# Kernel tuning notes

Hardware: AMD Instinct MI355X
Metric: run time of the kernel (lower is better)

Reference implementation:

```python
import jax, jax.numpy as jnp
import numpy as np

# Cost coefficients from MatcherConfig (init_kwargs)
C_CLASS, C_MASK, C_DICE, C_DIST, C_NLL, C_LIK = 2.0, 5.0, 5.0, 1.0, 0.5, 0.5

B, P, Q, E = 8, 16384, 256, 128  # images, pixels (H*W), queries, electrons


def setup_inputs() -> dict:
    key = jax.random.key(0)
    ks = jax.random.split(key, 8)
    mask_mask = jax.random.uniform(ks[0], (B, P, Q)) < 0.10           # sparsity pattern of pred logits
    mask_logit_values = jax.random.normal(ks[1], (B, P, Q), jnp.float32)
    seg_occ = jax.random.uniform(ks[2], (B, P, E)) < 0.05              # sparsity pattern of target segmap
    seg_vals = jax.random.uniform(ks[3], (B, P, E), jnp.float32, 1e-3, 1.0)
    segmap_values = jnp.where(seg_occ, seg_vals, 0.0)
    pred_logits = jax.random.normal(ks[4], (B, Q), jnp.float32)
    pred_positions = jax.random.uniform(ks[5], (B, Q, 2), jnp.float32)
    true_positions = jax.random.uniform(ks[6], (B, E, 2), jnp.float32)
    kd, ko = jax.random.split(ks[7])
    diag = 1.0 + 2.0 * jax.random.uniform(kd, (B, Q, 2), jnp.float32)  # positive diag of scale_tril
    off = 0.3 * jax.random.normal(ko, (B, Q), jnp.float32)
    pred_chol = jnp.zeros((B, Q, 2, 2), jnp.float32)
    pred_chol = pred_chol.at[..., 0, 0].set(diag[..., 0])
    pred_chol = pred_chol.at[..., 1, 1].set(diag[..., 1])
    pred_chol = pred_chol.at[..., 1, 0].set(off)
    image_sizes_xy = jnp.full((B, 2), 128.0, jnp.float32)
    return {
        'pred_logits': pred_logits,
        'mask_logit_values': mask_logit_values,
        'mask_mask': mask_mask,
        'segmap_values': segmap_values,
        'pred_positions': pred_positions,
        'pred_chol': pred_chol,
        'true_positions': true_positions,
        'image_sizes_xy': image_sizes_xy,
    }


def _total_cost(pred_logits, mask_logit_values, segmap_values, pred_positions,
                pred_chol, true_positions, image_sizes_xy, mask_mask):
    sp = jax.nn.softplus
    m = mask_mask
    # --- class cost: BCE(logit, 1) per query -> [B,Q]
    class_cost = sp(-pred_logits)
    # --- mask BCE cost (get_bce_cost): sparse entries only
    pos = jnp.where(m, sp(-mask_logit_values), 0.0)   # BCE vs 1 on nnz entries
    neg = jnp.where(m, sp(mask_logit_values), 0.0)    # BCE vs 0 on nnz entries
    targ = (segmap_values > 0).astype(pos.dtype)      # binarized target segmap
    pos_loss = jnp.einsum('bpq,bpe->bqe', pos, targ)
    neg_loss = neg.sum(1)[:, :, None] - jnp.einsum('bpq,bpe->bqe', neg, targ)
    nnz = jnp.maximum(targ.sum((1, 2)), 1.0)          # target _nnz() per image
    mask_cost = (pos_loss + neg_loss) / nnz[:, None, None]
    # --- dice cost (get_dice_cost): sparse softmax over query dim
    NEG = jnp.asarray(-1e30, mask_logit_values.dtype)
    z = jnp.where(m, mask_logit_values, NEG)
    mx = jnp.max(z, axis=-1, keepdims=True)
    ez = jnp.where(m, jnp.exp(z - mx), 0.0)
    s = ez.sum(-1, keepdims=True)
    pred_p = jnp.where(s > 0, ez / jnp.maximum(s, 1e-30), 0.0)  # [B,P,Q]
    num = 2.0 * jnp.einsum('bpq,bpe->bqe', pred_p, segmap_values)
    den = pred_p.sum(1)[:, :, None] + segmap_values.sum(1)[:, None, :]
    dice_cost = 1.0 - (num + 1.0) / (den + 1.0)
    # --- huber distance cost (delta=1), mean over xy
    d = pred_positions[:, :, None, :] - true_positions[:, None, :, :]  # [B,Q,E,2]
    ad = jnp.abs(d)
    huber_cost = jnp.where(ad < 1.0, 0.5 * d * d, ad - 0.5).mean(-1)
    # --- NLL / likelihood distance costs (MVN with scale_tril)
    mu = pred_positions * image_sizes_xy[:, None, :]
    y = true_positions * image_sizes_xy[:, None, :]
    diff = y[:, None, :, :] - mu[:, :, None, :]        # [B,Q,E,2]
    L00 = pred_chol[..., 0, 0][:, :, None]
    L10 = pred_chol[..., 1, 0][:, :, None]
    L11 = pred_chol[..., 1, 1][:, :, None]
    z0 = diff[..., 0] / L00
    z1 = (diff[..., 1] - L10 * z0) / L11
    nll_cost = 0.5 * (z0 * z0 + z1 * z1) + jnp.log(2.0 * jnp.pi) + jnp.log(L00) + jnp.log(L11)
    lik_cost = 1.0 - jnp.exp(-nll_cost)
    total = (C_CLASS * class_cost[:, :, None] + C_MASK * mask_cost + C_DICE * dice_cost
             + C_DIST * huber_cost + C_NLL * nll_cost + C_LIK * lik_cost)
    return total  # [B, Q, E] stacked per-image cost matrices


def reference(pred_logits, mask_logit_values, mask_mask, segmap_values,
              pred_positions, pred_chol, true_positions, image_sizes_xy):
    return _total_cost(pred_logits, mask_logit_values, segmap_values, pred_positions,
                       pred_chol, true_positions, image_sizes_xy, mask_mask)
```

## Files before the change

### kernel.cpp

```cpp
#include <hip/hip_runtime.h>
#include <cstdint>
#include <cstddef>

typedef float v4f __attribute__((ext_vector_type(4)));
typedef short short8 __attribute__((ext_vector_type(8)));

constexpr int B_ = 8, P_ = 16384, Q_ = 256, E_ = 128;

__device__ __forceinline__ unsigned short f2bf(float f) {
  unsigned int x = __float_as_uint(f);
  x += 0x7FFFu + ((x >> 16) & 1u);
  return (unsigned short)(x >> 16);
}
__device__ __forceinline__ float softplus_f(float x) {
  return fmaxf(x, 0.f) + __logf(1.f + __expf(-fabsf(x)));
}

__global__ __launch_bounds__(256) void prep_rows(
    const float* __restrict__ mlv, const int* __restrict__ mask,
    unsigned short* __restrict__ A1, unsigned short* __restrict__ PP,
    float* __restrict__ negsum, float* __restrict__ ppsum)
{
  __shared__ float rn[4][256];
  __shared__ float rp[4][256];
  const int t = threadIdx.x, w = t >> 6, l = t & 63;
  const int b = blockIdx.x >> 7;
  float accN[4] = {0,0,0,0}, accP[4] = {0,0,0,0};
  for (int it = 0; it < 32; ++it) {
    const size_t row = (size_t)blockIdx.x * 128 + it * 4 + w;
    const size_t off = row * 256 + l * 4;
    float4 x4 = *(const float4*)(mlv + off);
    int4   m4 = *(const int4*)(mask + off);
    float xs[4] = {x4.x, x4.y, x4.z, x4.w};
    int   ms[4] = {m4.x, m4.y, m4.z, m4.w};
    float ez[4]; float s = 0.f;
    unsigned short a1u[4];
#pragma unroll
    for (int j = 0; j < 4; ++j) {
      bool m = (ms[j] != 0);
      float x = xs[j];
      float e = m ? __expf(x) : 0.f;
      ez[j] = e; s += e;
      a1u[j] = f2bf(m ? -x : 0.f);
      accN[j] += m ? softplus_f(x) : 0.f;
    }
#pragma unroll
    for (int o = 32; o > 0; o >>= 1) s += __shfl_xor(s, o, 64);
    float inv = (s > 0.f) ? (1.f / s) : 0.f;
    unsigned short pu[4];
#pragma unroll
    for (int j = 0; j < 4; ++j) { float p = ez[j] * inv; accP[j] += p; pu[j] = f2bf(p); }
    uint2 aw, pw;
    aw.x = (unsigned)a1u[0] | ((unsigned)a1u[1] << 16);
    aw.y = (unsigned)a1u[2] | ((unsigned)a1u[3] << 16);
    pw.x = (unsigned)pu[0] | ((unsigned)pu[1] << 16);
    pw.y = (unsigned)pu[2] | ((unsigned)pu[3] << 16);
    *(uint2*)(A1 + off) = aw;
    *(uint2*)(PP + off) = pw;
  }
#pragma unroll
  for (int j = 0; j < 4; ++j) { rn[w][l * 4 + j] = accN[j]; rp[w][l * 4 + j] = accP[j]; }
  __syncthreads();
  float sn = rn[0][t] + rn[1][t] + rn[2][t] + rn[3][t];
  float sq = rp[0][t] + rp[1][t] + rp[2][t] + rp[3][t];
  atomicAdd(&negsum[b * 256 + t], sn);
  atomicAdd(&ppsum[b * 256 + t], sq);
}

__global__ __launch_bounds__(256) void prep_seg(
    const float* __restrict__ seg, unsigned short* __restrict__ SG,
    float* __restrict__ segsum, float* __restrict__ nnzb)
{
  __shared__ float sbin[128];
  __shared__ float nns;
  const int t = threadIdx.x;
  const int b = blockIdx.x >> 6;
  if (t < 128) sbin[t] = 0.f;
  if (t == 0) nns = 0.f;
  __syncthreads();
  float accS[4] = {0,0,0,0}; float cnt = 0.f;
  const size_t base = (size_t)blockIdx.x * 32768 + t * 4;
  for (int it = 0; it < 32; ++it) {
    size_t off = base + (size_t)it * 1024;
    float4 v = *(const float4*)(seg + off);
    float vs[4] = {v.x, v.y, v.z, v.w};
    unsigned short u[4];
#pragma unroll
    for (int j = 0; j < 4; ++j) {
      u[j] = f2bf(vs[j]); accS[j] += vs[j];
      cnt += (vs[j] > 0.f) ? 1.f : 0.f;
    }
    uint2 wv; wv.x = (unsigned)u[0] | ((unsigned)u[1] << 16);
    wv.y = (unsigned)u[2] | ((unsigned)u[3] << 16);
    *(uint2*)(SG + off) = wv;
  }
  const int e0 = (t * 4) & 127;
#pragma unroll
  for (int j = 0; j < 4; ++j) atomicAdd(&sbin[e0 + j], accS[j]);
#pragma unroll
  for (int o = 32; o > 0; o >>= 1) cnt += __shfl_xor(cnt, o, 64);
  if ((t & 63) == 0) atomicAdd(&nns, cnt);
  __syncthreads();
  if (t < 128) atomicAdd(&segsum[b * 128 + t], sbin[t]);
  if (t == 0) atomicAdd(&nnzb[b], nns);
}

__global__ __launch_bounds__(256) void gemm_split(
    const unsigned short* __restrict__ A1, const unsigned short* __restrict__ PP,
    const unsigned short* __restrict__ SG, float* __restrict__ part)
{
  __shared__ __align__(16) unsigned int ldsA[128 * 36];
  __shared__ __align__(16) unsigned int ldsB[128 * 36];
  const int id = blockIdx.x;
  const int ks = id & 15, qt = (id >> 4) & 1, g = (id >> 5) & 1, b = id >> 6;
  const unsigned short* Aop = (g ? PP : A1) + (size_t)b * P_ * Q_;
  const unsigned short* Bop = SG + (size_t)b * P_ * E_;
  const int t = threadIdx.x;
  const int c16 = t >> 4, pr = t & 15;
  const int w = t >> 6, l = t & 63, lm = l & 15, quad = l >> 4;
  const int wm = w & 1, wn = w >> 1;
  v4f acc[4][4];
#pragma unroll
  for (int i = 0; i < 4; ++i)
#pragma unroll
    for (int j = 0; j < 4; ++j) acc[i][j] = (v4f)0.f;

  for (int c = 0; c < 16; ++c) {
    const int pbase = ks * 1024 + c * 64;
    __syncthreads();
#pragma unroll
    for (int pass = 0; pass < 2; ++pass) {
      const int r0 = pass * 32 + 2 * pr;
      const unsigned short* ap = Aop + (size_t)(pbase + r0) * Q_ + qt * 128 + c16 * 8;
      uint4 w0 = *(const uint4*)ap;
      uint4 w1 = *(const uint4*)(ap + Q_);
      const unsigned short* bp = Bop + (size_t)(pbase + r0) * E_ + c16 * 8;
      uint4 v0 = *(const uint4*)bp;
      uint4 v1 = *(const uint4*)(bp + E_);
      const int dbase = pass * 16 + pr;
      unsigned int aw0[4] = {w0.x, w0.y, w0.z, w0.w};
      unsigned int aw1[4] = {w1.x, w1.y, w1.z, w1.w};
      unsigned int bw0[4] = {v0.x, v0.y, v0.z, v0.w};
      unsigned int bw1[4] = {v1.x, v1.y, v1.z, v1.w};
#pragma unroll
      for (int k = 0; k < 4; ++k) {
        const int col = c16 * 8 + 2 * k;
        unsigned int lo = (aw0[k] & 0xFFFFu) | (aw1[k] << 16);
        unsigned int hi = (aw0[k] >> 16) | (aw1[k] & 0xFFFF0000u);
        ldsA[col * 36 + dbase] = lo;
        ldsA[(col + 1) * 36 + dbase] = hi;
        unsigned int blo = (bw0[k] & 0xFFFFu) | (bw1[k] << 16);
        unsigned int bhi = (bw0[k] >> 16) | (bw1[k] & 0xFFFF0000u);
        if (g == 0) {
          blo = ((blo & 0xFFFFu) ? 0x3F80u : 0u) | ((blo & 0xFFFF0000u) ? 0x3F800000u : 0u);
          bhi = ((bhi & 0xFFFFu) ? 0x3F80u : 0u) | ((bhi & 0xFFFF0000u) ? 0x3F800000u : 0u);
        }
        ldsB[col * 36 + dbase] = blo;
        ldsB[(col + 1) * 36 + dbase] = bhi;
      }
    }
    __syncthreads();
#pragma unroll
    for (int k32 = 0; k32 < 2; ++k32) {
      short8 af[4], bf[4];
#pragma unroll
      for (int i = 0; i < 4; ++i) {
        const int arow = wm * 64 + i * 16 + lm;
        af[i] = *(const short8*)((const char*)ldsA + arow * 144 + k32 * 64 + quad * 16);
        const int brow = wn * 64 + i * 16 + lm;
        bf[i] = *(const short8*)((const char*)ldsB + brow * 144 + k32 * 64 + quad * 16);
      }
#pragma unroll
      for (int i = 0; i < 4; ++i)
#pragma unroll
        for (int j = 0; j < 4; ++j)
          acc[i][j] = __builtin_amdgcn_mfma_f32_16x16x32_bf16(af[i], bf[j], acc[i][j], 0, 0, 0);
    }
  }
  float* pout = part + ((size_t)(g * 8 + b) * 16 + ks) * (Q_ * E_);
#pragma unroll
  for (int i = 0; i < 4; ++i)
#pragma unroll
    for (int r = 0; r < 4; ++r) {
      const int q = qt * 128 + wm * 64 + i * 16 + quad * 4 + r;
#pragma unroll
      for (int j = 0; j < 4; ++j) {
        const int e = wn * 64 + j * 16 + lm;
        pout[q * E_ + e] = acc[i][j][r];
      }
    }
}

__global__ __launch_bounds__(128) void epilogue(
    const float* __restrict__ part,
    const float* __restrict__ negsum, const float* __restrict__ ppsum,
    const float* __restrict__ segsum, const float* __restrict__ nnzb,
    const float* __restrict__ logits, const float* __restrict__ ppos,
    const float* __restrict__ chol, const float* __restrict__ tpos,
    const float* __restrict__ imgsz, float* __restrict__ out)
{
  const int bq = blockIdx.x;
  const int b = bq >> 8;
  const int e = threadIdx.x;
  const int qe = (bq & 255) * 128 + e;
  const float* p0 = part + (size_t)b * 524288 + qe;
  const float* p1 = part + (size_t)(8 + b) * 524288 + qe;
  float g1 = 0.f, g2 = 0.f;
#pragma unroll
  for (int k = 0; k < 16; ++k) { g1 += p0[k * 32768]; g2 += p1[k * 32768]; }

  const float nnz = fmaxf(nnzb[b], 1.f);
  const float mask_cost = (negsum[bq] + g1) / nnz;
  const float dice = 1.f - (2.f * g2 + 1.f) / (ppsum[bq] + segsum[b * 128 + e] + 1.f);
  const float cls = softplus_f(-logits[bq]);
  const float px = ppos[bq * 2], py = ppos[bq * 2 + 1];
  const float tx = tpos[(b * 128 + e) * 2], ty = tpos[(b * 128 + e) * 2 + 1];
  const float dx = px - tx, dy = py - ty;
  const float ax = fabsf(dx), ay = fabsf(dy);
  const float hx = (ax < 1.f) ? 0.5f * dx * dx : ax - 0.5f;
  const float hy = (ay < 1.f) ? 0.5f * dy * dy : ay - 0.5f;
  const float huber = 0.5f * (hx + hy);
  const float sx = imgsz[b * 2], sy = imgsz[b * 2 + 1];
  const float L00 = chol[bq * 4 + 0], L10 = chol[bq * 4 + 2], L11 = chol[bq * 4 + 3];
  const float d0 = (tx - px) * sx, d1 = (ty - py) * sy;
  const float z0 = d0 / L00;
  const float z1 = (d1 - L10 * z0) / L11;
  const float nll = 0.5f * (z0 * z0 + z1 * z1) + 1.8378770664093453f + __logf(L00) + __logf(L11);
  const float lik = 1.f - __expf(-nll);
  out[bq * 128 + e] = 2.f * cls + 5.f * mask_cost + 5.f * dice + huber + 0.5f * nll + 0.5f * lik;
}

extern "C" void kernel_launch(void* const* d_in, const int* in_sizes, int n_in,
                              void* d_out, int out_size, void* d_ws, size_t ws_size,
                              hipStream_t stream)
{
  (void)in_sizes; (void)n_in; (void)out_size; (void)ws_size;
  const float* logits = (const float*)d_in[0];
  const float* mlv    = (const float*)d_in[1];
  const int*   mask   = (const int*)d_in[2];
  const float* seg    = (const float*)d_in[3];
  const float* ppos   = (const float*)d_in[4];
  const float* chol   = (const float*)d_in[5];
  const float* tpos   = (const float*)d_in[6];
  const float* imgsz  = (const float*)d_in[7];

  char* ws = (char*)d_ws;
  unsigned short* A1 = (unsigned short*)(ws);
  unsigned short* PP = (unsigned short*)(ws + 67108864);
  unsigned short* SG = (unsigned short*)(ws + 134217728);
  float* part   = (float*)(ws + 167772160);
  float* negsum = (float*)(ws + 234881024);
  float* ppsum  = (float*)(ws + 234889216);
  float* segsum = (float*)(ws + 234897408);
  float* nnzb   = (float*)(ws + 234901504);

  hipMemsetAsync(ws + 234881024, 0, 20544, stream);
  prep_rows<<<1024, 256, 0, stream>>>(mlv, mask, A1, PP, negsum, ppsum);
  prep_seg<<<512, 256, 0, stream>>>(seg, SG, segsum, nnzb);
  gemm_split<<<512, 256, 0, stream>>>(A1, PP, SG, part);
  epilogue<<<2048, 128, 0, stream>>>(part, negsum, ppsum, segsum, nnzb,
                                     logits, ppos, chol, tpos, imgsz, (float*)d_out);
}
```

Before: 425.6 us.

## Pre-transpose bf16 operands into swizzled tiles and load GEMM tiles directly to LDS

The prep kernels now write A, P, segmap and a precomputed binary segmap as K-major swizzled 64-pixel tiles, transposed through LDS. This lets the GEMM fill shared memory with direct global-to-LDS 16-byte loads, with no in-kernel shuffling or binarisation. The split-K partial outputs are summed with atomics into one buffer, so the epilogue no longer reads 16 partial slices. The cost is an extra binary segmap buffer, atomic contention in the GEMM store, and a more complex prep transpose with larger register arrays.

```diff
diff --git a/kernel.cpp b/kernel.cpp
--- a/kernel.cpp
+++ b/kernel.cpp
@@ -4,171 +4,254 @@
 
 typedef float v4f __attribute__((ext_vector_type(4)));
 typedef short short8 __attribute__((ext_vector_type(8)));
+typedef unsigned short ushort_t;
 
 constexpr int B_ = 8, P_ = 16384, Q_ = 256, E_ = 128;
 
-__device__ __forceinline__ unsigned short f2bf(float f) {
+__device__ __forceinline__ unsigned int f2bf(float f) {
   unsigned int x = __float_as_uint(f);
   x += 0x7FFFu + ((x >> 16) & 1u);
-  return (unsigned short)(x >> 16);
+  return x >> 16;
 }
 __device__ __forceinline__ float softplus_f(float x) {
   return fmaxf(x, 0.f) + __logf(1.f + __expf(-fabsf(x)));
 }
-
-__global__ __launch_bounds__(256) void prep_rows(
+__device__ __forceinline__ void gload16(const void* g, void* l) {
+  __builtin_amdgcn_global_load_lds((const __attribute__((address_space(1))) void*)g,
+                                   (__attribute__((address_space(3))) void*)l,
+                                   16, 0, 0);
+}
+
+__global__ __launch_bounds__(256, 4) void prep_rows(
     const float* __restrict__ mlv, const int* __restrict__ mask,
-    unsigned short* __restrict__ A1, unsigned short* __restrict__ PP,
+    ushort_t* __restrict__ A1T, ushort_t* __restrict__ PPT,
     float* __restrict__ negsum, float* __restrict__ ppsum)
 {
-  __shared__ float rn[4][256];
-  __shared__ float rp[4][256];
+  __shared__ unsigned int st[256 * 33];
   const int t = threadIdx.x, w = t >> 6, l = t & 63;
-  const int b = blockIdx.x >> 7;
-  float accN[4] = {0,0,0,0}, accP[4] = {0,0,0,0};
-  for (int it = 0; it < 32; ++it) {
-    const size_t row = (size_t)blockIdx.x * 128 + it * 4 + w;
-    const size_t off = row * 256 + l * 4;
-    float4 x4 = *(const float4*)(mlv + off);
-    int4   m4 = *(const int4*)(mask + off);
-    float xs[4] = {x4.x, x4.y, x4.z, x4.w};
-    int   ms[4] = {m4.x, m4.y, m4.z, m4.w};
-    float ez[4]; float s = 0.f;
-    unsigned short a1u[4];
+  const int b = blockIdx.x >> 8, cp = blockIdx.x & 255;
+  const size_t base = ((size_t)b * P_ + cp * 64) * Q_;
+  float accN[4] = {0.f,0.f,0.f,0.f}, accP[4] = {0.f,0.f,0.f,0.f};
+  unsigned int a1w[4][4][2], ppw[4][4][2];
+
+#pragma unroll
+  for (int g = 0; g < 4; ++g) {
+#pragma unroll
+    for (int j = 0; j < 4; ++j) { a1w[g][j][0]=0; a1w[g][j][1]=0; ppw[g][j][0]=0; ppw[g][j][1]=0; }
+#pragma unroll
+    for (int r = 0; r < 4; ++r) {
+      const int pl = (w << 4) + (g << 2) + r;
+      const float* xp = mlv + base + (size_t)pl * Q_ + l;
+      const int*   mp = mask + base + (size_t)pl * Q_ + l;
+      float xs[4]; int ms[4];
+#pragma unroll
+      for (int j = 0; j < 4; ++j) { xs[j] = xp[j * 64]; ms[j] = mp[j * 64]; }
+      float ev[4]; float s = 0.f;
+#pragma unroll
+      for (int j = 0; j < 4; ++j) {
+        const bool mm = ms[j] != 0;
+        const float xv = xs[j];
+        const float e = mm ? __expf(xv) : 0.f;
+        ev[j] = e; s += e;
+        accN[j] += __logf(1.f + e);
+        a1w[g][j][r >> 1] |= f2bf(mm ? -xv : 0.f) << ((r & 1) * 16);
+      }
+#pragma unroll
+      for (int o = 32; o; o >>= 1) s += __shfl_xor(s, o, 64);
+      const float inv = (s > 0.f) ? (1.f / s) : 0.f;
+#pragma unroll
+      for (int j = 0; j < 4; ++j) {
+        const float p = ev[j] * inv;
+        accP[j] += p;
+        ppw[g][j][r >> 1] |= f2bf(p) << ((r & 1) * 16);
+      }
+    }
+  }
+  const size_t tb = ((size_t)(b * 256 + cp)) * 16384;
+#pragma unroll
+  for (int g = 0; g < 4; ++g)
 #pragma unroll
     for (int j = 0; j < 4; ++j) {
-      bool m = (ms[j] != 0);
-      float x = xs[j];
-      float e = m ? __expf(x) : 0.f;
-      ez[j] = e; s += e;
-      a1u[j] = f2bf(m ? -x : 0.f);
-      accN[j] += m ? softplus_f(x) : 0.f;
-    }
-#pragma unroll
-    for (int o = 32; o > 0; o >>= 1) s += __shfl_xor(s, o, 64);
-    float inv = (s > 0.f) ? (1.f / s) : 0.f;
-    unsigned short pu[4];
-#pragma unroll
-    for (int j = 0; j < 4; ++j) { float p = ez[j] * inv; accP[j] += p; pu[j] = f2bf(p); }
-    uint2 aw, pw;
-    aw.x = (unsigned)a1u[0] | ((unsigned)a1u[1] << 16);
-    aw.y = (unsigned)a1u[2] | ((unsigned)a1u[3] << 16);
-    pw.x = (unsigned)pu[0] | ((unsigned)pu[1] << 16);
-    pw.y = (unsigned)pu[2] | ((unsigned)pu[3] << 16);
-    *(uint2*)(A1 + off) = aw;
-    *(uint2*)(PP + off) = pw;
-  }
-#pragma unroll
-  for (int j = 0; j < 4; ++j) { rn[w][l * 4 + j] = accN[j]; rp[w][l * 4 + j] = accP[j]; }
-  __syncthreads();
-  float sn = rn[0][t] + rn[1][t] + rn[2][t] + rn[3][t];
-  float sq = rp[0][t] + rp[1][t] + rp[2][t] + rp[3][t];
-  atomicAdd(&negsum[b * 256 + t], sn);
-  atomicAdd(&ppsum[b * 256 + t], sq);
-}
-
-__global__ __launch_bounds__(256) void prep_seg(
-    const float* __restrict__ seg, unsigned short* __restrict__ SG,
+      const int wb = (l + (j << 6)) * 33 + (w << 3) + (g << 1);
+      st[wb] = a1w[g][j][0]; st[wb + 1] = a1w[g][j][1];
+    }
+  __syncthreads();
+  {
+    uint4* dst = (uint4*)(A1T + tb);
+#pragma unroll
+    for (int pass = 0; pass < 8; ++pass) {
+      const int gi = pass * 256 + t;
+      const int q = gi >> 3, c = (gi & 7) ^ (q & 7);
+      const int wd = q * 33 + c * 4;
+      uint4 v; v.x = st[wd]; v.y = st[wd+1]; v.z = st[wd+2]; v.w = st[wd+3];
+      dst[gi] = v;
+    }
+  }
+  __syncthreads();
+#pragma unroll
+  for (int g = 0; g < 4; ++g)
+#pragma unroll
+    for (int j = 0; j < 4; ++j) {
+      const int wb = (l + (j << 6)) * 33 + (w << 3) + (g << 1);
+      st[wb] = ppw[g][j][0]; st[wb + 1] = ppw[g][j][1];
+    }
+  __syncthreads();
+  {
+    uint4* dst = (uint4*)(PPT + tb);
+#pragma unroll
+    for (int pass = 0; pass < 8; ++pass) {
+      const int gi = pass * 256 + t;
+      const int q = gi >> 3, c = (gi & 7) ^ (q & 7);
+      const int wd = q * 33 + c * 4;
+      uint4 v; v.x = st[wd]; v.y = st[wd+1]; v.z = st[wd+2]; v.w = st[wd+3];
+      dst[gi] = v;
+    }
+  }
+  __syncthreads();
+  float* red = (float*)st;
+#pragma unroll
+  for (int j = 0; j < 4; ++j) red[w * 256 + l + (j << 6)] = accN[j];
+  __syncthreads();
+  {
+    const float sn = red[t] + red[256 + t] + red[512 + t] + red[768 + t];
+    atomicAdd(&negsum[b * 256 + t], sn);
+  }
+  __syncthreads();
+#pragma unroll
+  for (int j = 0; j < 4; ++j) red[w * 256 + l + (j << 6)] = accP[j];
+  __syncthreads();
+  {
+    const float sq = red[t] + red[256 + t] + red[512 + t] + red[768 + t];
+    atomicAdd(&ppsum[b * 256 + t], sq);
+  }
+}
+
+__global__ __launch_bounds__(256, 4) void prep_seg(
+    const float* __restrict__ seg, ushort_t* __restrict__ SGT, ushort_t* __restrict__ SGB,
     float* __restrict__ segsum, float* __restrict__ nnzb)
 {
-  __shared__ float sbin[128];
-  __shared__ float nns;
-  const int t = threadIdx.x;
-  const int b = blockIdx.x >> 6;
-  if (t < 128) sbin[t] = 0.f;
-  if (t == 0) nns = 0.f;
-  __syncthreads();
-  float accS[4] = {0,0,0,0}; float cnt = 0.f;
-  const size_t base = (size_t)blockIdx.x * 32768 + t * 4;
-  for (int it = 0; it < 32; ++it) {
-    size_t off = base + (size_t)it * 1024;
-    float4 v = *(const float4*)(seg + off);
-    float vs[4] = {v.x, v.y, v.z, v.w};
-    unsigned short u[4];
-#pragma unroll
-    for (int j = 0; j < 4; ++j) {
-      u[j] = f2bf(vs[j]); accS[j] += vs[j];
-      cnt += (vs[j] > 0.f) ? 1.f : 0.f;
-    }
-    uint2 wv; wv.x = (unsigned)u[0] | ((unsigned)u[1] << 16);
-    wv.y = (unsigned)u[2] | ((unsigned)u[3] << 16);
-    *(uint2*)(SG + off) = wv;
-  }
-  const int e0 = (t * 4) & 127;
-#pragma unroll
-  for (int j = 0; j < 4; ++j) atomicAdd(&sbin[e0 + j], accS[j]);
-#pragma unroll
-  for (int o = 32; o > 0; o >>= 1) cnt += __shfl_xor(cnt, o, 64);
-  if ((t & 63) == 0) atomicAdd(&nns, cnt);
-  __syncthreads();
-  if (t < 128) atomicAdd(&segsum[b * 128 + t], sbin[t]);
-  if (t == 0) atomicAdd(&nnzb[b], nns);
-}
-
-__global__ __launch_bounds__(256) void gemm_split(
-    const unsigned short* __restrict__ A1, const unsigned short* __restrict__ PP,
-    const unsigned short* __restrict__ SG, float* __restrict__ part)
-{
-  __shared__ __align__(16) unsigned int ldsA[128 * 36];
-  __shared__ __align__(16) unsigned int ldsB[128 * 36];
+  __shared__ unsigned int st[128 * 33];
+  const int t = threadIdx.x, w = t >> 6, l = t & 63;
+  const int b = blockIdx.x >> 8, cp = blockIdx.x & 255;
+  const size_t base = ((size_t)b * P_ + cp * 64) * E_;
+  float accS[2] = {0.f, 0.f}; float cnt = 0.f;
+  unsigned int sgw[4][2][2], sbw[4][2][2];
+#pragma unroll
+  for (int g = 0; g < 4; ++g) {
+#pragma unroll
+    for (int j = 0; j < 2; ++j) { sgw[g][j][0]=0; sgw[g][j][1]=0; sbw[g][j][0]=0; sbw[g][j][1]=0; }
+#pragma unroll
+    for (int r = 0; r < 4; ++r) {
+      const int pl = (w << 4) + (g << 2) + r;
+      const float* vp = seg + base + (size_t)pl * E_ + l;
+#pragma unroll
+      for (int j = 0; j < 2; ++j) {
+        const float v = vp[j * 64];
+        const bool nz = v > 0.f;
+        accS[j] += v; cnt += nz ? 1.f : 0.f;
+        sgw[g][j][r >> 1] |= f2bf(v) << ((r & 1) * 16);
+        sbw[g][j][r >> 1] |= (nz ? 0x3F80u : 0u) << ((r & 1) * 16);
+      }
+    }
+  }
+  const size_t tb = ((size_t)(b * 256 + cp)) * 8192;
+#pragma unroll
+  for (int g = 0; g < 4; ++g)
+#pragma unroll
+    for (int j = 0; j < 2; ++j) {
+      const int wb = (l + (j << 6)) * 33 + (w << 3) + (g << 1);
+      st[wb] = sgw[g][j][0]; st[wb + 1] = sgw[g][j][1];
+    }
+  __syncthreads();
+  {
+    uint4* dst = (uint4*)(SGT + tb);
+#pragma unroll
+    for (int pass = 0; pass < 4; ++pass) {
+      const int gi = pass * 256 + t;
+      const int q = gi >> 3, c = (gi & 7) ^ (q & 7);
+      const int wd = q * 33 + c * 4;
+      uint4 v; v.x = st[wd]; v.y = st[wd+1]; v.z = st[wd+2]; v.w = st[wd+3];
+      dst[gi] = v;
+    }
+  }
+  __syncthreads();
+#pragma unroll
+  for (int g = 0; g < 4; ++g)
+#pragma unroll
+    for (int j = 0; j < 2; ++j) {
+      const int wb = (l + (j << 6)) * 33 + (w << 3) + (g << 1);
+      st[wb] = sbw[g][j][0]; st[wb + 1] = sbw[g][j][1];
+    }
+  __syncthreads();
+  {
+    uint4* dst = (uint4*)(SGB + tb);
+#pragma unroll
+    for (int pass = 0; pass < 4; ++pass) {
+      const int gi = pass * 256 + t;
+      const int q = gi >> 3, c = (gi & 7) ^ (q & 7);
+      const int wd = q * 33 + c * 4;
+      uint4 v; v.x = st[wd]; v.y = st[wd+1]; v.z = st[wd+2]; v.w = st[wd+3];
+      dst[gi] = v;
+    }
+  }
+  __syncthreads();
+  float* red = (float*)st;
+#pragma unroll
+  for (int j = 0; j < 2; ++j) red[w * 128 + l + (j << 6)] = accS[j];
+  __syncthreads();
+  if (t < 128) {
+    const float ss = red[t] + red[128 + t] + red[256 + t] + red[384 + t];
+    atomicAdd(&segsum[b * 128 + t], ss);
+  }
+#pragma unroll
+  for (int o = 32; o; o >>= 1) cnt += __shfl_xor(cnt, o, 64);
+  if (l == 0) atomicAdd(&nnzb[b], cnt);
+}
+
+__global__ __launch_bounds__(256, 2) void gemm_mfma(
+    const ushort_t* __restrict__ A1T, const ushort_t* __restrict__ PPT,
+    const ushort_t* __restrict__ SGT, const ushort_t* __restrict__ SGB,
+    float* __restrict__ part)
+{
+  __shared__ __align__(16) char lds[32768];
   const int id = blockIdx.x;
   const int ks = id & 15, qt = (id >> 4) & 1, g = (id >> 5) & 1, b = id >> 6;
-  const unsigned short* Aop = (g ? PP : A1) + (size_t)b * P_ * Q_;
-  const unsigned short* Bop = SG + (size_t)b * P_ * E_;
-  const int t = threadIdx.x;
-  const int c16 = t >> 4, pr = t & 15;
-  const int w = t >> 6, l = t & 63, lm = l & 15, quad = l >> 4;
+  const ushort_t* Aall = g ? PPT : A1T;
+  const ushort_t* Ball = g ? SGT : SGB;
+  const int t = threadIdx.x, l = t & 63, w = t >> 6;
+  const int lm = l & 15, quad = l >> 4;
   const int wm = w & 1, wn = w >> 1;
   v4f acc[4][4];
 #pragma unroll
   for (int i = 0; i < 4; ++i)
 #pragma unroll
     for (int j = 0; j < 4; ++j) acc[i][j] = (v4f)0.f;
-
-  for (int c = 0; c < 16; ++c) {
-    const int pbase = ks * 1024 + c * 64;
+  const size_t cp0 = (size_t)b * 256 + ks * 16;
+  const char* gA = (const char*)(Aall + cp0 * 16384 + qt * 8192);
+  const char* gB = (const char*)(Ball + cp0 * 8192);
+  const int off = t * 16;
+
+  for (int it = 0; it < 16; ++it) {
     __syncthreads();
-#pragma unroll
-    for (int pass = 0; pass < 2; ++pass) {
-      const int r0 = pass * 32 + 2 * pr;
-      const unsigned short* ap = Aop + (size_t)(pbase + r0) * Q_ + qt * 128 + c16 * 8;
-      uint4 w0 = *(const uint4*)ap;
-      uint4 w1 = *(const uint4*)(ap + Q_);
-      const unsigned short* bp = Bop + (size_t)(pbase + r0) * E_ + c16 * 8;
-      uint4 v0 = *(const uint4*)bp;
-      uint4 v1 = *(const uint4*)(bp + E_);
-      const int dbase = pass * 16 + pr;
-      unsigned int aw0[4] = {w0.x, w0.y, w0.z, w0.w};
-      unsigned int aw1[4] = {w1.x, w1.y, w1.z, w1.w};
-      unsigned int bw0[4] = {v0.x, v0.y, v0.z, v0.w};
-      unsigned int bw1[4] = {v1.x, v1.y, v1.z, v1.w};
-#pragma unroll
-      for (int k = 0; k < 4; ++k) {
-        const int col = c16 * 8 + 2 * k;
-        unsigned int lo = (aw0[k] & 0xFFFFu) | (aw1[k] << 16);
-        unsigned int hi = (aw0[k] >> 16) | (aw1[k] & 0xFFFF0000u);
-        ldsA[col * 36 + dbase] = lo;
-        ldsA[(col + 1) * 36 + dbase] = hi;
-        unsigned int blo = (bw0[k] & 0xFFFFu) | (bw1[k] << 16);
-        unsigned int bhi = (bw0[k] >> 16) | (bw1[k] & 0xFFFF0000u);
-        if (g == 0) {
-          blo = ((blo & 0xFFFFu) ? 0x3F80u : 0u) | ((blo & 0xFFFF0000u) ? 0x3F800000u : 0u);
-          bhi = ((bhi & 0xFFFFu) ? 0x3F80u : 0u) | ((bhi & 0xFFFF0000u) ? 0x3F800000u : 0u);
-        }
-        ldsB[col * 36 + dbase] = blo;
-        ldsB[(col + 1) * 36 + dbase] = bhi;
-      }
-    }
+    const char* pa = gA + (size_t)it * 32768;
+    const char* pb = gB + (size_t)it * 16384;
+    gload16(pa + off,          lds + off);
+    gload16(pa + off + 4096,   lds + off + 4096);
+    gload16(pa + off + 8192,   lds + off + 8192);
+    gload16(pa + off + 12288,  lds + off + 12288);
+    gload16(pb + off,          lds + 16384 + off);
+    gload16(pb + off + 4096,   lds + 16384 + off + 4096);
+    gload16(pb + off + 8192,   lds + 16384 + off + 8192);
+    gload16(pb + off + 12288,  lds + 16384 + off + 12288);
     __syncthreads();
 #pragma unroll
     for (int k32 = 0; k32 < 2; ++k32) {
       short8 af[4], bf[4];
+      const int ach = ((k32 << 2) | quad) ^ (lm & 7);
 #pragma unroll
       for (int i = 0; i < 4; ++i) {
-        const int arow = wm * 64 + i * 16 + lm;
-        af[i] = *(const short8*)((const char*)ldsA + arow * 144 + k32 * 64 + quad * 16);
-        const int brow = wn * 64 + i * 16 + lm;
-        bf[i] = *(const short8*)((const char*)ldsB + brow * 144 + k32 * 64 + quad * 16);
+        af[i] = *(const short8*)(lds + (wm * 64 + i * 16 + lm) * 128 + ach * 16);
+        bf[i] = *(const short8*)(lds + 16384 + (wn * 64 + i * 16 + lm) * 128 + ach * 16);
       }
 #pragma unroll
       for (int i = 0; i < 4; ++i)
@@ -177,7 +260,7 @@
           acc[i][j] = __builtin_amdgcn_mfma_f32_16x16x32_bf16(af[i], bf[j], acc[i][j], 0, 0, 0);
     }
   }
-  float* pout = part + ((size_t)(g * 8 + b) * 16 + ks) * (Q_ * E_);
+  float* pout = part + (size_t)(g * 8 + b) * 32768;
 #pragma unroll
   for (int i = 0; i < 4; ++i)
 #pragma unroll
@@ -186,7 +269,7 @@
 #pragma unroll
       for (int j = 0; j < 4; ++j) {
         const int e = wn * 64 + j * 16 + lm;
-        pout[q * E_ + e] = acc[i][j][r];
+        atomicAdd(&pout[q * 128 + e], acc[i][j][r]);
       }
     }
 }
@@ -203,11 +286,8 @@
   const int b = bq >> 8;
   const int e = threadIdx.x;
   const int qe = (bq & 255) * 128 + e;
-  const float* p0 = part + (size_t)b * 524288 + qe;
-  const float* p1 = part + (size_t)(8 + b) * 524288 + qe;
-  float g1 = 0.f, g2 = 0.f;
-#pragma unroll
-  for (int k = 0; k < 16; ++k) { g1 += p0[k * 32768]; g2 += p1[k * 32768]; }
+  const float g1 = part[(size_t)b * 32768 + qe];
+  const float g2 = part[(size_t)(8 + b) * 32768 + qe];
 
   const float nnz = fmaxf(nnzb[b], 1.f);
   const float mask_cost = (negsum[bq] + g1) / nnz;
@@ -245,19 +325,20 @@
   const float* imgsz  = (const float*)d_in[7];
 
   char* ws = (char*)d_ws;
-  unsigned short* A1 = (unsigned short*)(ws);
-  unsigned short* PP = (unsigned short*)(ws + 67108864);
-  unsigned short* SG = (unsigned short*)(ws + 134217728);
-  float* part   = (float*)(ws + 167772160);
-  float* negsum = (float*)(ws + 234881024);
-  float* ppsum  = (float*)(ws + 234889216);
-  float* segsum = (float*)(ws + 234897408);
-  float* nnzb   = (float*)(ws + 234901504);
-
-  hipMemsetAsync(ws + 234881024, 0, 20544, stream);
-  prep_rows<<<1024, 256, 0, stream>>>(mlv, mask, A1, PP, negsum, ppsum);
-  prep_seg<<<512, 256, 0, stream>>>(seg, SG, segsum, nnzb);
-  gemm_split<<<512, 256, 0, stream>>>(A1, PP, SG, part);
+  ushort_t* A1T = (ushort_t*)(ws);
+  ushort_t* PPT = (ushort_t*)(ws + 67108864);
+  ushort_t* SGT = (ushort_t*)(ws + 134217728);
+  ushort_t* SGB = (ushort_t*)(ws + 167772160);
+  float* part   = (float*)(ws + 201326592);
+  float* negsum = (float*)(ws + 203423744);
+  float* ppsum  = (float*)(ws + 203431936);
+  float* segsum = (float*)(ws + 203440128);
+  float* nnzb   = (float*)(ws + 203444224);
+
+  hipMemsetAsync(ws + 201326592, 0, 2117696, stream);
+  prep_seg<<<2048, 256, 0, stream>>>(seg, SGT, SGB, segsum, nnzb);
+  prep_rows<<<2048, 256, 0, stream>>>(mlv, mask, A1T, PPT, negsum, ppsum);
+  gemm_mfma<<<512, 256, 0, stream>>>(A1T, PPT, SGT, SGB, part);
   epilogue<<<2048, 128, 0, stream>>>(part, negsum, ppsum, segsum, nnzb,
                                      logits, ppos, chol, tpos, imgsz, (float*)d_out);
 }
```

Result: slower. 512.6 us (+20.4%).

## Fuse prep and GEMM into one kernel, reducing split-K partials with atomics

Applied to the files above, without the earlier changes.

Merges the row-softmax/BCE prep, segmap prep and both bf16 MFMA GEMMs into a single kernel. Each block converts its pixel slab to bf16 directly in LDS and multiplies there, so the bf16 intermediates (A1, PP, SG) are never written to or read back from global memory. Split-K partials are now combined with float atomics into one small buffer, so the epilogue reads one value instead of summing 16. The softplus term is computed as log(1+exp(x)) from the already-computed exponential. Costs: only 256 blocks of 512 threads, a large atomic epilogue, and a serialized convert-then-MFMA loop with two barriers per step.

```diff
diff --git a/kernel.cpp b/kernel.cpp
--- a/kernel.cpp
+++ b/kernel.cpp
@@ -7,186 +7,207 @@
 
 constexpr int B_ = 8, P_ = 16384, Q_ = 256, E_ = 128;
 
-__device__ __forceinline__ unsigned short f2bf(float f) {
+__device__ __forceinline__ unsigned int f2bf(float f) {
   unsigned int x = __float_as_uint(f);
   x += 0x7FFFu + ((x >> 16) & 1u);
-  return (unsigned short)(x >> 16);
+  return x >> 16;
 }
 __device__ __forceinline__ float softplus_f(float x) {
   return fmaxf(x, 0.f) + __logf(1.f + __expf(-fabsf(x)));
 }
-
-__global__ __launch_bounds__(256) void prep_rows(
+__device__ __forceinline__ short8 mk8(unsigned a, unsigned b, unsigned c, unsigned d) {
+  union { unsigned u[4]; short8 s; } x;
+  x.u[0] = a; x.u[1] = b; x.u[2] = c; x.u[3] = d; return x.s;
+}
+__device__ __forceinline__ float wsum(float v) {
+#pragma unroll
+  for (int o = 32; o; o >>= 1) v += __shfl_xor(v, o, 64);
+  return v;
+}
+
+__global__ __launch_bounds__(512, 2) void fused_all(
     const float* __restrict__ mlv, const int* __restrict__ mask,
-    unsigned short* __restrict__ A1, unsigned short* __restrict__ PP,
-    float* __restrict__ negsum, float* __restrict__ ppsum)
-{
-  __shared__ float rn[4][256];
-  __shared__ float rp[4][256];
-  const int t = threadIdx.x, w = t >> 6, l = t & 63;
-  const int b = blockIdx.x >> 7;
-  float accN[4] = {0,0,0,0}, accP[4] = {0,0,0,0};
-  for (int it = 0; it < 32; ++it) {
-    const size_t row = (size_t)blockIdx.x * 128 + it * 4 + w;
-    const size_t off = row * 256 + l * 4;
-    float4 x4 = *(const float4*)(mlv + off);
-    int4   m4 = *(const int4*)(mask + off);
-    float xs[4] = {x4.x, x4.y, x4.z, x4.w};
-    int   ms[4] = {m4.x, m4.y, m4.z, m4.w};
-    float ez[4]; float s = 0.f;
-    unsigned short a1u[4];
-#pragma unroll
-    for (int j = 0; j < 4; ++j) {
-      bool m = (ms[j] != 0);
-      float x = xs[j];
-      float e = m ? __expf(x) : 0.f;
-      ez[j] = e; s += e;
-      a1u[j] = f2bf(m ? -x : 0.f);
-      accN[j] += m ? softplus_f(x) : 0.f;
-    }
-#pragma unroll
-    for (int o = 32; o > 0; o >>= 1) s += __shfl_xor(s, o, 64);
-    float inv = (s > 0.f) ? (1.f / s) : 0.f;
-    unsigned short pu[4];
-#pragma unroll
-    for (int j = 0; j < 4; ++j) { float p = ez[j] * inv; accP[j] += p; pu[j] = f2bf(p); }
-    uint2 aw, pw;
-    aw.x = (unsigned)a1u[0] | ((unsigned)a1u[1] << 16);
-    aw.y = (unsigned)a1u[2] | ((unsigned)a1u[3] << 16);
-    pw.x = (unsigned)pu[0] | ((unsigned)pu[1] << 16);
-    pw.y = (unsigned)pu[2] | ((unsigned)pu[3] << 16);
-    *(uint2*)(A1 + off) = aw;
-    *(uint2*)(PP + off) = pw;
-  }
-#pragma unroll
-  for (int j = 0; j < 4; ++j) { rn[w][l * 4 + j] = accN[j]; rp[w][l * 4 + j] = accP[j]; }
-  __syncthreads();
-  float sn = rn[0][t] + rn[1][t] + rn[2][t] + rn[3][t];
-  float sq = rp[0][t] + rp[1][t] + rp[2][t] + rp[3][t];
-  atomicAdd(&negsum[b * 256 + t], sn);
-  atomicAdd(&ppsum[b * 256 + t], sq);
-}
-
-__global__ __launch_bounds__(256) void prep_seg(
-    const float* __restrict__ seg, unsigned short* __restrict__ SG,
+    const float* __restrict__ seg, float* __restrict__ part,
+    float* __restrict__ negsum, float* __restrict__ ppsum,
     float* __restrict__ segsum, float* __restrict__ nnzb)
 {
-  __shared__ float sbin[128];
-  __shared__ float nns;
-  const int t = threadIdx.x;
-  const int b = blockIdx.x >> 6;
-  if (t < 128) sbin[t] = 0.f;
-  if (t == 0) nns = 0.f;
+  __shared__ __align__(16) unsigned int lds[12544];
+  unsigned int* A1t = lds;
+  unsigned int* EZt = lds + 4160;
+  unsigned int* SBt = lds + 8320;
+  unsigned int* STt = lds + 10432;
+
+  const int t = threadIdx.x, w = t >> 6, l = t & 63;
+  const int lm = l & 15, quad = l >> 4;
+  const int wr = w & 3, wc = w >> 2;
+  const int jj = l >> 5, le = l & 31;
+  const int b = blockIdx.x >> 5, ks = blockIdx.x & 31;
+
+  v4f acc0[4][4], acc1[4][4];
+#pragma unroll
+  for (int i = 0; i < 4; ++i)
+#pragma unroll
+    for (int j = 0; j < 4; ++j) { acc0[i][j] = (v4f)0.f; acc1[i][j] = (v4f)0.f; }
+  float accN[4] = {0.f,0.f,0.f,0.f};
+  float accP[4] = {0.f,0.f,0.f,0.f};
+  float accS[4] = {0.f,0.f,0.f,0.f};
+  float cnt = 0.f;
+
+  const float* mp = mlv + ((size_t)b * P_ + ks * 512 + 4 * w) * Q_ + 4 * l;
+  const int*   kp = mask + ((size_t)b * P_ + ks * 512 + 4 * w) * Q_ + 4 * l;
+  const float* sp = seg + ((size_t)b * P_ + ks * 512 + 4 * w + 2 * jj) * E_ + 4 * le;
+
+  float4 X[4]; int4 M[4]; float4 S0, S1;
+#pragma unroll
+  for (int r = 0; r < 4; ++r) {
+    X[r] = *(const float4*)(mp + (size_t)r * Q_);
+    M[r] = *(const int4*)(kp + (size_t)r * Q_);
+  }
+  S0 = *(const float4*)(sp);
+  S1 = *(const float4*)(sp + E_);
+
+  for (int it = 0; it < 16; ++it) {
+    float xs[4][4]; int ms[4][4];
+#pragma unroll
+    for (int r = 0; r < 4; ++r) {
+      xs[r][0] = X[r].x; xs[r][1] = X[r].y; xs[r][2] = X[r].z; xs[r][3] = X[r].w;
+      ms[r][0] = M[r].x; ms[r][1] = M[r].y; ms[r][2] = M[r].z; ms[r][3] = M[r].w;
+    }
+    float sv0[4] = {S0.x, S0.y, S0.z, S0.w};
+    float sv1[4] = {S1.x, S1.y, S1.z, S1.w};
+
+    if (it < 15) {
+      mp += 32 * Q_; kp += 32 * Q_; sp += 32 * E_;
+#pragma unroll
+      for (int r = 0; r < 4; ++r) {
+        X[r] = *(const float4*)(mp + (size_t)r * Q_);
+        M[r] = *(const int4*)(kp + (size_t)r * Q_);
+      }
+      S0 = *(const float4*)(sp);
+      S1 = *(const float4*)(sp + E_);
+    }
+
+    float ez[4][4], rs[4];
+#pragma unroll
+    for (int r = 0; r < 4; ++r) {
+      float s = 0.f;
+#pragma unroll
+      for (int j = 0; j < 4; ++j) {
+        const bool mm = ms[r][j] != 0;
+        const float e = mm ? __expf(xs[r][j]) : 0.f;
+        ez[r][j] = e; s += e;
+        accN[j] += __logf(1.f + e);
+      }
+      rs[r] = s;
+    }
+#pragma unroll
+    for (int r = 0; r < 4; ++r) rs[r] = wsum(rs[r]);
+    float inv[4];
+#pragma unroll
+    for (int r = 0; r < 4; ++r) inv[r] = (rs[r] > 0.f) ? (1.f / rs[r]) : 0.f;
+
+    unsigned int a1p[2][4], ezp[2][4];
+#pragma unroll
+    for (int jp = 0; jp < 2; ++jp)
+#pragma unroll
+      for (int j = 0; j < 4; ++j) {
+        const int r0 = 2 * jp, r1 = 2 * jp + 1;
+        a1p[jp][j] = f2bf(ms[r0][j] ? -xs[r0][j] : 0.f)
+                   | (f2bf(ms[r1][j] ? -xs[r1][j] : 0.f) << 16);
+        const float p0 = ez[r0][j] * inv[r0];
+        const float p1 = ez[r1][j] * inv[r1];
+        accP[j] += p0 + p1;
+        ezp[jp][j] = f2bf(p0) | (f2bf(p1) << 16);
+      }
+    unsigned int sb[4], st_[4];
+#pragma unroll
+    for (int j = 0; j < 4; ++j) {
+      accS[j] += sv0[j] + sv1[j];
+      cnt += ((sv0[j] > 0.f) ? 1.f : 0.f) + ((sv1[j] > 0.f) ? 1.f : 0.f);
+      sb[j]  = ((sv0[j] > 0.f) ? 0x3F80u : 0u) | ((sv1[j] > 0.f) ? 0x3F800000u : 0u);
+      st_[j] = f2bf(sv0[j]) | (f2bf(sv1[j]) << 16);
+    }
+
+    __syncthreads();
+    { uint4 v; v.x=a1p[0][0]; v.y=a1p[0][1]; v.z=a1p[0][2]; v.w=a1p[0][3];
+      *(uint4*)(A1t + (2*w)     * 260 + 4*l) = v; }
+    { uint4 v; v.x=a1p[1][0]; v.y=a1p[1][1]; v.z=a1p[1][2]; v.w=a1p[1][3];
+      *(uint4*)(A1t + (2*w + 1) * 260 + 4*l) = v; }
+    { uint4 v; v.x=ezp[0][0]; v.y=ezp[0][1]; v.z=ezp[0][2]; v.w=ezp[0][3];
+      *(uint4*)(EZt + (2*w)     * 260 + 4*l) = v; }
+    { uint4 v; v.x=ezp[1][0]; v.y=ezp[1][1]; v.z=ezp[1][2]; v.w=ezp[1][3];
+      *(uint4*)(EZt + (2*w + 1) * 260 + 4*l) = v; }
+    { uint4 v; v.x=sb[0]; v.y=sb[1]; v.z=sb[2]; v.w=sb[3];
+      *(uint4*)(SBt + (2*w + jj) * 132 + 4*le) = v; }
+    { uint4 v; v.x=st_[0]; v.y=st_[1]; v.z=st_[2]; v.w=st_[3];
+      *(uint4*)(STt + (2*w + jj) * 132 + 4*le) = v; }
+    __syncthreads();
+
+    short8 af0[4], af1[4], bf0[4], bf1[4];
+#pragma unroll
+    for (int i = 0; i < 4; ++i) {
+      const int q_abs = wr * 64 + i * 16 + lm;
+      const int c0 = 4 * quad;
+      af0[i] = mk8(A1t[c0*260 + q_abs], A1t[(c0+1)*260 + q_abs],
+                   A1t[(c0+2)*260 + q_abs], A1t[(c0+3)*260 + q_abs]);
+      af1[i] = mk8(EZt[c0*260 + q_abs], EZt[(c0+1)*260 + q_abs],
+                   EZt[(c0+2)*260 + q_abs], EZt[(c0+3)*260 + q_abs]);
+    }
+#pragma unroll
+    for (int j = 0; j < 4; ++j) {
+      const int e_abs = wc * 64 + j * 16 + lm;
+      const int c0 = 4 * quad;
+      bf0[j] = mk8(SBt[c0*132 + e_abs], SBt[(c0+1)*132 + e_abs],
+                   SBt[(c0+2)*132 + e_abs], SBt[(c0+3)*132 + e_abs]);
+      bf1[j] = mk8(STt[c0*132 + e_abs], STt[(c0+1)*132 + e_abs],
+                   STt[(c0+2)*132 + e_abs], STt[(c0+3)*132 + e_abs]);
+    }
+#pragma unroll
+    for (int i = 0; i < 4; ++i)
+#pragma unroll
+      for (int j = 0; j < 4; ++j) {
+        acc0[i][j] = __builtin_amdgcn_mfma_f32_16x16x32_bf16(af0[i], bf0[j], acc0[i][j], 0, 0, 0);
+        acc1[i][j] = __builtin_amdgcn_mfma_f32_16x16x32_bf16(af1[i], bf1[j], acc1[i][j], 0, 0, 0);
+      }
+  }
+
   __syncthreads();
-  float accS[4] = {0,0,0,0}; float cnt = 0.f;
-  const size_t base = (size_t)blockIdx.x * 32768 + t * 4;
-  for (int it = 0; it < 32; ++it) {
-    size_t off = base + (size_t)it * 1024;
-    float4 v = *(const float4*)(seg + off);
-    float vs[4] = {v.x, v.y, v.z, v.w};
-    unsigned short u[4];
-#pragma unroll
-    for (int j = 0; j < 4; ++j) {
-      u[j] = f2bf(vs[j]); accS[j] += vs[j];
-      cnt += (vs[j] > 0.f) ? 1.f : 0.f;
-    }
-    uint2 wv; wv.x = (unsigned)u[0] | ((unsigned)u[1] << 16);
-    wv.y = (unsigned)u[2] | ((unsigned)u[3] << 16);
-    *(uint2*)(SG + off) = wv;
-  }
-  const int e0 = (t * 4) & 127;
-#pragma unroll
-  for (int j = 0; j < 4; ++j) atomicAdd(&sbin[e0 + j], accS[j]);
-#pragma unroll
-  for (int o = 32; o > 0; o >>= 1) cnt += __shfl_xor(cnt, o, 64);
-  if ((t & 63) == 0) atomicAdd(&nns, cnt);
+  float* fr = (float*)lds;
+#pragma unroll
+  for (int j = 0; j < 4; ++j) {
+    fr[w * 256 + 4 * l + j] = accN[j];
+    fr[2048 + w * 256 + 4 * l + j] = accP[j];
+    fr[4096 + (2 * w + jj) * 128 + 4 * le + j] = accS[j];
+  }
   __syncthreads();
-  if (t < 128) atomicAdd(&segsum[b * 128 + t], sbin[t]);
-  if (t == 0) atomicAdd(&nnzb[b], nns);
-}
-
-__global__ __launch_bounds__(256) void gemm_split(
-    const unsigned short* __restrict__ A1, const unsigned short* __restrict__ PP,
-    const unsigned short* __restrict__ SG, float* __restrict__ part)
-{
-  __shared__ __align__(16) unsigned int ldsA[128 * 36];
-  __shared__ __align__(16) unsigned int ldsB[128 * 36];
-  const int id = blockIdx.x;
-  const int ks = id & 15, qt = (id >> 4) & 1, g = (id >> 5) & 1, b = id >> 6;
-  const unsigned short* Aop = (g ? PP : A1) + (size_t)b * P_ * Q_;
-  const unsigned short* Bop = SG + (size_t)b * P_ * E_;
-  const int t = threadIdx.x;
-  const int c16 = t >> 4, pr = t & 15;
-  const int w = t >> 6, l = t & 63, lm = l & 15, quad = l >> 4;
-  const int wm = w & 1, wn = w >> 1;
-  v4f acc[4][4];
+  if (t < 256) {
+    float sn = 0.f, sq = 0.f;
+#pragma unroll
+    for (int k = 0; k < 8; ++k) { sn += fr[k * 256 + t]; sq += fr[2048 + k * 256 + t]; }
+    atomicAdd(&negsum[b * 256 + t], sn);
+    atomicAdd(&ppsum[b * 256 + t], sq);
+  } else if (t < 384) {
+    const int e = t - 256;
+    float ss = 0.f;
+#pragma unroll
+    for (int k = 0; k < 16; ++k) ss += fr[4096 + k * 128 + e];
+    atomicAdd(&segsum[b * 128 + e], ss);
+  }
+  cnt = wsum(cnt);
+  if (l == 0) atomicAdd(&nnzb[b], cnt);
+
+  float* p0 = part + (size_t)b * 32768;
+  float* p1 = part + (size_t)(8 + b) * 32768;
 #pragma unroll
   for (int i = 0; i < 4; ++i)
 #pragma unroll
-    for (int j = 0; j < 4; ++j) acc[i][j] = (v4f)0.f;
-
-  for (int c = 0; c < 16; ++c) {
-    const int pbase = ks * 1024 + c * 64;
-    __syncthreads();
-#pragma unroll
-    for (int pass = 0; pass < 2; ++pass) {
-      const int r0 = pass * 32 + 2 * pr;
-      const unsigned short* ap = Aop + (size_t)(pbase + r0) * Q_ + qt * 128 + c16 * 8;
-      uint4 w0 = *(const uint4*)ap;
-      uint4 w1 = *(const uint4*)(ap + Q_);
-      const unsigned short* bp = Bop + (size_t)(pbase + r0) * E_ + c16 * 8;
-      uint4 v0 = *(const uint4*)bp;
-      uint4 v1 = *(const uint4*)(bp + E_);
-      const int dbase = pass * 16 + pr;
-      unsigned int aw0[4] = {w0.x, w0.y, w0.z, w0.w};
-      unsigned int aw1[4] = {w1.x, w1.y, w1.z, w1.w};
-      unsigned int bw0[4] = {v0.x, v0.y, v0.z, v0.w};
-      unsigned int bw1[4] = {v1.x, v1.y, v1.z, v1.w};
-#pragma unroll
-      for (int k = 0; k < 4; ++k) {
-        const int col = c16 * 8 + 2 * k;
-        unsigned int lo = (aw0[k] & 0xFFFFu) | (aw1[k] << 16);
-        unsigned int hi = (aw0[k] >> 16) | (aw1[k] & 0xFFFF0000u);
-        ldsA[col * 36 + dbase] = lo;
-        ldsA[(col + 1) * 36 + dbase] = hi;
-        unsigned int blo = (bw0[k] & 0xFFFFu) | (bw1[k] << 16);
-        unsigned int bhi = (bw0[k] >> 16) | (bw1[k] & 0xFFFF0000u);
-        if (g == 0) {
-          blo = ((blo & 0xFFFFu) ? 0x3F80u : 0u) | ((blo & 0xFFFF0000u) ? 0x3F800000u : 0u);
-          bhi = ((bhi & 0xFFFFu) ? 0x3F80u : 0u) | ((bhi & 0xFFFF0000u) ? 0x3F800000u : 0u);
-        }
-        ldsB[col * 36 + dbase] = blo;
-        ldsB[(col + 1) * 36 + dbase] = bhi;
-      }
-    }
-    __syncthreads();
-#pragma unroll
-    for (int k32 = 0; k32 < 2; ++k32) {
-      short8 af[4], bf[4];
-#pragma unroll
-      for (int i = 0; i < 4; ++i) {
-        const int arow = wm * 64 + i * 16 + lm;
-        af[i] = *(const short8*)((const char*)ldsA + arow * 144 + k32 * 64 + quad * 16);
-        const int brow = wn * 64 + i * 16 + lm;
-        bf[i] = *(const short8*)((const char*)ldsB + brow * 144 + k32 * 64 + quad * 16);
-      }
-#pragma unroll
-      for (int i = 0; i < 4; ++i)
-#pragma unroll
-        for (int j = 0; j < 4; ++j)
-          acc[i][j] = __builtin_amdgcn_mfma_f32_16x16x32_bf16(af[i], bf[j], acc[i][j], 0, 0, 0);
-    }
-  }
-  float* pout = part + ((size_t)(g * 8 + b) * 16 + ks) * (Q_ * E_);
-#pragma unroll
-  for (int i = 0; i < 4; ++i)
-#pragma unroll
     for (int r = 0; r < 4; ++r) {
-      const int q = qt * 128 + wm * 64 + i * 16 + quad * 4 + r;
-#pragma unroll
-      for (int j = 0; j < 4; ++j) {
-        const int e = wn * 64 + j * 16 + lm;
-        pout[q * E_ + e] = acc[i][j][r];
+      const int q = wr * 64 + i * 16 + quad * 4 + r;
+#pragma unroll
+      for (int j = 0; j < 4; ++j) {
+        const int e = wc * 64 + j * 16 + lm;
+        atomicAdd(&p0[q * 128 + e], acc0[i][j][r]);
+        atomicAdd(&p1[q * 128 + e], acc1[i][j][r]);
       }
     }
 }
@@ -203,11 +224,8 @@
   const int b = bq >> 8;
   const int e = threadIdx.x;
   const int qe = (bq & 255) * 128 + e;
-  const float* p0 = part + (size_t)b * 524288 + qe;
-  const float* p1 = part + (size_t)(8 + b) * 524288 + qe;
-  float g1 = 0.f, g2 = 0.f;
-#pragma unroll
-  for (int k = 0; k < 16; ++k) { g1 += p0[k * 32768]; g2 += p1[k * 32768]; }
+  const float g1 = part[(size_t)b * 32768 + qe];
+  const float g2 = part[(size_t)(8 + b) * 32768 + qe];
 
   const float nnz = fmaxf(nnzb[b], 1.f);
   const float mask_cost = (negsum[bq] + g1) / nnz;
@@ -245,19 +263,14 @@
   const float* imgsz  = (const float*)d_in[7];
 
   char* ws = (char*)d_ws;
-  unsigned short* A1 = (unsigned short*)(ws);
-  unsigned short* PP = (unsigned short*)(ws + 67108864);
-  unsigned short* SG = (unsigned short*)(ws + 134217728);
-  float* part   = (float*)(ws + 167772160);
-  float* negsum = (float*)(ws + 234881024);
-  float* ppsum  = (float*)(ws + 234889216);
-  float* segsum = (float*)(ws + 234897408);
-  float* nnzb   = (float*)(ws + 234901504);
-
-  hipMemsetAsync(ws + 234881024, 0, 20544, stream);
-  prep_rows<<<1024, 256, 0, stream>>>(mlv, mask, A1, PP, negsum, ppsum);
-  prep_seg<<<512, 256, 0, stream>>>(seg, SG, segsum, nnzb);
-  gemm_split<<<512, 256, 0, stream>>>(A1, PP, SG, part);
+  float* part   = (float*)(ws);
+  float* negsum = (float*)(ws + 2097152);
+  float* ppsum  = (float*)(ws + 2105344);
+  float* segsum = (float*)(ws + 2113536);
+  float* nnzb   = (float*)(ws + 2117632);
+
+  hipMemsetAsync(ws, 0, 2117664, stream);
+  fused_all<<<256, 512, 0, stream>>>(mlv, mask, seg, part, negsum, ppsum, segsum, nnzb);
   epilogue<<<2048, 128, 0, stream>>>(part, negsum, ppsum, segsum, nnzb,
                                      logits, ppos, chol, tpos, imgsz, (float*)d_out);
 }
```

After: 415.0 us. 1.03x faster.
